# Kernel optimization log

Hardware: AMD Instinct MI355X
Metric: run time of the kernel (lower is better)

## Reference

```python
import jax, jax.numpy as jnp
import numpy as np

HID = 768
INTER = 3072
H = 12
DH = 64
N = 16384
W = 256   # attention_width
L = 512   # per-sequence length (power of 2, used via the uint32 bit-mask trick)


def rotate_every_two(x):
    x1 = x[..., ::2]
    x2 = x[..., 1::2]
    return jnp.stack((-x2, x1), axis=-1).reshape(x.shape)


def setup_inputs() -> dict:
    key = jax.random.key(0)
    ks = jax.random.split(key, 6)
    # GPT-J style interleaved rotary tables: sin/cos each value repeated twice
    inv_freq = 1.0 / (10000.0 ** (np.arange(0, DH, 2) / DH))  # [DH/2]
    ang = np.arange(N)[:, None] * inv_freq[None, :]           # [N, DH/2]
    pos_sin = jnp.asarray(np.repeat(np.sin(ang), 2, axis=-1), dtype=jnp.float32)
    pos_cos = jnp.asarray(np.repeat(np.cos(ang), 2, axis=-1), dtype=jnp.float32)
    return {
        "x": jax.random.normal(ks[0], (N, HID), dtype=jnp.float32),
        "normed_ages": jax.random.normal(ks[1], (N,), dtype=jnp.float32),
        "pos_sin": pos_sin,
        "pos_cos": pos_cos,
        "ln_scale": jnp.ones((HID,), dtype=jnp.float32),
        "ln_offset": jnp.zeros((HID,), dtype=jnp.float32),
        "w_in": jax.random.normal(ks[2], (HID, 3 * HID + INTER), dtype=jnp.float32) * 0.02,
        "b_in": jnp.zeros((3 * HID + INTER,), dtype=jnp.float32),
        "w_out": jax.random.normal(ks[3], (HID + INTER, HID), dtype=jnp.float32) * 0.02,
        "b_out": jnp.zeros((HID,), dtype=jnp.float32),
        "length": L,
    }


def reference(x, normed_ages, pos_sin, pos_cos, ln_scale, ln_offset,
              w_in, b_in, w_out, b_out, length):
    # LayerNorm (haiku: eps=1e-5, create_scale/offset)
    mu = jnp.mean(x, axis=-1, keepdims=True)
    var = jnp.var(x, axis=-1, keepdims=True)
    xn = (x - mu) * jax.lax.rsqrt(var + 1e-5) * ln_scale + ln_offset

    # fused QKV + FF projection (note: original computes x_with_ages but never uses it)
    mid = xn @ w_in + b_in
    q, k, v, ff = jnp.split(mid, [HID, 2 * HID, 3 * HID], axis=-1)

    def to_heads(t):  # [N, HID] -> [H, N, DH]
        return t.reshape(N, H, DH).transpose(1, 0, 2)

    q, k, v = to_heads(q), to_heads(k), to_heads(v)

    # rotary ('per_head'): sincos broadcast over heads
    sin, cos = pos_sin[None], pos_cos[None]
    q = q * cos + rotate_every_two(q) * sin
    k = k * cos + rotate_every_two(k) * sin

    # local (sliding-window, causal, within-sequence) attention, chunked by W
    C = W
    nc = N // C
    qc = q.reshape(H, nc, C, DH)
    kc = k.reshape(H, nc, C, DH)
    vc = v.reshape(H, nc, C, DH)
    kprev = jnp.concatenate([jnp.zeros_like(kc[:, :1]), kc[:, :-1]], axis=1)
    vprev = jnp.concatenate([jnp.zeros_like(vc[:, :1]), vc[:, :-1]], axis=1)
    kcat = jnp.concatenate([kprev, kc], axis=2)  # [H, nc, 2C, DH]
    vcat = jnp.concatenate([vprev, vc], axis=2)

    qi = (jnp.arange(nc) * C)[:, None] + jnp.arange(C)        # [nc, C]
    kj = (jnp.arange(nc) * C)[:, None] - C + jnp.arange(2 * C)  # [nc, 2C]
    lm = ~(jnp.uint32(length) - jnp.uint32(1))  # same bit-trick as the module
    same_seq = ((qi[:, :, None].astype(jnp.uint32) & lm) ==
                (jnp.maximum(kj, 0)[:, None, :].astype(jnp.uint32) & lm))
    d = qi[:, :, None] - kj[:, None, :]
    mask = (kj[:, None, :] >= 0) & (d >= 0) & (d < W) & same_seq  # [nc, C, 2C]

    scale = 1.0 / jnp.sqrt(jnp.float32(DH))
    scores = jnp.einsum('hncd,hnkd->hnck', qc, kcat) * scale
    scores = jnp.where(mask[None], scores, jnp.float32(-1e30))
    probs = jax.nn.softmax(scores, axis=-1)
    attn = jnp.einsum('hnck,hnkd->hncd', probs, vcat)

    attn = attn.reshape(H, N, DH).transpose(1, 0, 2).reshape(N, HID)
    combined = jnp.concatenate([attn, jax.nn.gelu(ff)], axis=-1)
    return xn + combined @ w_out + b_out
```

## Files before the change

kernel.cpp:

```cpp
#include <hip/hip_runtime.h>

#define N_TOK 16384
#define HIDN  768
#define MIDN  5376
#define COMBN 3840
#define NH    12
#define DHD   64
#define CHUNK 256
#define WIN   256

typedef short s16x8 __attribute__((ext_vector_type(8)));
typedef short s16x4 __attribute__((ext_vector_type(4)));
typedef float f32x4 __attribute__((ext_vector_type(4)));

__device__ __forceinline__ float bf2f(unsigned short u){
  union { unsigned u; float f; } x; x.u = ((unsigned)u) << 16; return x.f;
}
__device__ __forceinline__ unsigned short f2bf(float f){
  union { float f; unsigned u; } x; x.f = f;
  unsigned r = x.u + 0x7fffu + ((x.u >> 16) & 1u);
  return (unsigned short)(r >> 16);
}
__device__ __forceinline__ float gelu_fast(float x){
  float u = -1.5957691216057308f * (x + 0.044715f * x * x * x);
  return x / (1.f + __expf(u));
}
__device__ __forceinline__ void glds16(const void* g, void* l){
  __builtin_amdgcn_global_load_lds(
      (const __attribute__((address_space(1))) unsigned*)g,
      (__attribute__((address_space(3))) unsigned*)l, 16, 0, 0);
}

__global__ __launch_bounds__(256) void transpose_f2b(
    const float* __restrict__ in, unsigned short* __restrict__ out,
    int R, int Cc)
{
  __shared__ short t[64 * 72];
  const int tid = threadIdx.x;
  const int r0 = blockIdx.y * 64, c0 = blockIdx.x * 64;
  #pragma unroll
  for (int rep = 0; rep < 4; rep++){
    int v = tid + 256 * rep;
    int r = v >> 4, s = v & 15;
    float4 d = *(const float4*)(in + (size_t)(r0 + r) * Cc + c0 + s * 4);
    s16x4 o = { (short)f2bf(d.x), (short)f2bf(d.y), (short)f2bf(d.z), (short)f2bf(d.w) };
    *(s16x4*)(t + r * 72 + s * 4) = o;
  }
  __syncthreads();
  #pragma unroll
  for (int rep = 0; rep < 2; rep++){
    int v = tid + 256 * rep;
    int c = v & 63, s2 = v >> 6;
    s16x8 d;
    #pragma unroll
    for (int j = 0; j < 8; j++) d[j] = t[(s2 * 8 + j) * 72 + c];
    *(s16x8*)(out + (size_t)(c0 + c) * R + r0 + s2 * 8) = d;
  }
}

__global__ __launch_bounds__(256) void ln_kernel(
    const float* __restrict__ x, const float* __restrict__ sc,
    const float* __restrict__ ofs, unsigned short* __restrict__ xn)
{
  const int lane = threadIdx.x & 63, wv = threadIdx.x >> 6;
  const int row = blockIdx.x * 4 + wv;
  const float4* xr = (const float4*)(x + (size_t)row * HIDN);
  float4 vals[3];
  float sum = 0.f, sq = 0.f;
  #pragma unroll
  for (int j = 0; j < 3; j++){
    vals[j] = xr[lane + 64 * j];
    sum += vals[j].x + vals[j].y + vals[j].z + vals[j].w;
    sq  += vals[j].x * vals[j].x + vals[j].y * vals[j].y
         + vals[j].z * vals[j].z + vals[j].w * vals[j].w;
  }
  #pragma unroll
  for (int o = 1; o < 64; o <<= 1){ sum += __shfl_xor(sum, o); sq += __shfl_xor(sq, o); }
  const float mu = sum * (1.f / HIDN);
  const float rs = rsqrtf(fmaxf(sq * (1.f / HIDN) - mu * mu, 0.f) + 1e-5f);
  s16x4* xo = (s16x4*)(xn + (size_t)row * HIDN);
  const float4* scp = (const float4*)sc;
  const float4* ofp = (const float4*)ofs;
  #pragma unroll
  for (int j = 0; j < 3; j++){
    int p = lane + 64 * j;
    float4 s = scp[p], o = ofp[p];
    s16x4 w;
    w[0] = (short)f2bf((vals[j].x - mu) * rs * s.x + o.x);
    w[1] = (short)f2bf((vals[j].y - mu) * rs * s.y + o.y);
    w[2] = (short)f2bf((vals[j].z - mu) * rs * s.z + o.z);
    w[3] = (short)f2bf((vals[j].w - mu) * rs * s.w + o.w);
    xo[p] = w;
  }
}

template<int K>
__device__ __forceinline__ void gemm_pipe3(
    const unsigned short* __restrict__ A, const unsigned short* __restrict__ BT,
    short* SM,
    int tid, int quad, int l15, int wr, int wc, int m0, int n0,
    f32x4 acc[4][4])
{
  constexpr int T = K / 32;
  char* const SMc = (char*)SM;
  const int srow = tid >> 2;
  const int ksw  = ((tid & 3) ^ ((tid >> 3) & 3)) * 8;
  const unsigned short* Ap = A  + (size_t)(m0 + srow) * K + ksw;
  const unsigned short* Bp = BT + (size_t)(n0 + srow) * K + ksw;
  const size_t hstep = (size_t)64 * K;

  const int segx = ((quad ^ ((l15 >> 1) & 3)) << 4);
  int offA[4], offB[4];
  #pragma unroll
  for (int mf = 0; mf < 4; mf++) offA[mf] = (wr * 64 + mf * 16 + l15) * 64 + segx;
  #pragma unroll
  for (int nf = 0; nf < 4; nf++) offB[nf] = (wc * 64 + nf * 16 + l15) * 64 + segx;

  auto stage = [&](int tt){
    const int b = tt & 3;
    char* Ad = SMc + b * 16384 + tid * 16;
    char* Bd = SMc + b * 16384 + 8192 + tid * 16;
    glds16(Ap + tt * 32,         Ad);
    glds16(Ap + tt * 32 + hstep, Ad + 4096);
    glds16(Bp + tt * 32,         Bd);
    glds16(Bp + tt * 32 + hstep, Bd + 4096);
  };

  s16x8 af[4], bf[4];
  auto rdfrags = [&](int b){
    const char* Ab = SMc + b * 16384;
    const char* Bb = SMc + b * 16384 + 8192;
    #pragma unroll
    for (int i = 0; i < 4; i++) af[i] = *(const s16x8*)(Ab + offA[i]);
    #pragma unroll
    for (int j = 0; j < 4; j++) bf[j] = *(const s16x8*)(Bb + offB[j]);
  };

  stage(0); stage(1); stage(2); stage(3);
  asm volatile("s_waitcnt vmcnt(12)" ::: "memory");
  asm volatile("s_barrier" ::: "memory");
  rdfrags(0);

  #pragma unroll 4
  for (int t = 0; t < T; ++t){
    if (t + 4 < T) stage(t + 4);
    __builtin_amdgcn_s_setprio(1);
    #pragma unroll
    for (int i = 0; i < 4; i++)
      #pragma unroll
      for (int j = 0; j < 4; j++)
        acc[i][j] = __builtin_amdgcn_mfma_f32_16x16x32_bf16(af[i], bf[j], acc[i][j], 0, 0, 0);
    __builtin_amdgcn_s_setprio(0);
    if (t + 1 < T){
      if (t + 4 < T)      { asm volatile("s_waitcnt vmcnt(12)" ::: "memory"); }
      else if (t + 3 < T) { asm volatile("s_waitcnt vmcnt(8)"  ::: "memory"); }
      else if (t + 2 < T) { asm volatile("s_waitcnt vmcnt(4)"  ::: "memory"); }
      else                { asm volatile("s_waitcnt vmcnt(0)"  ::: "memory"); }
      asm volatile("s_barrier" ::: "memory");
      rdfrags((t + 1) & 3);
    }
  }
}

__global__ __launch_bounds__(256, 2) void gemm1_k(
    const unsigned short* __restrict__ A, const unsigned short* __restrict__ BT,
    const float* __restrict__ bias,
    const float* __restrict__ psin, const float* __restrict__ pcos,
    unsigned short* __restrict__ qb, unsigned short* __restrict__ kb,
    unsigned short* __restrict__ vb, unsigned short* __restrict__ comb)
{
  __shared__ short SM[32768];
  const int tid = threadIdx.x, lane = tid & 63, wv = tid >> 6;
  const int quad = lane >> 4, l15 = lane & 15;
  const int wr = wv >> 1, wc = wv & 1;

  const int nbx = gridDim.x;
  const int bid = blockIdx.x + blockIdx.y * nbx;
  const int GM = 16;
  const int group = bid / (GM * nbx);
  const int rem   = bid % (GM * nbx);
  const int m0 = (group * GM + (rem % GM)) * 128;
  const int n0 = (rem / GM) * 128;

  f32x4 acc[4][4];
  #pragma unroll
  for (int i = 0; i < 4; i++)
    #pragma unroll
    for (int j = 0; j < 4; j++) acc[i][j] = (f32x4){0.f,0.f,0.f,0.f};

  gemm_pipe3<HIDN>(A, BT, SM, tid, quad, l15, wr, wc, m0, n0, acc);

  unsigned short* dstb; int cb; int cls;
  if (n0 < 768)       { dstb = qb;   cb = n0;        cls = 0; }
  else if (n0 < 1536) { dstb = kb;   cb = n0 - 768;  cls = 1; }
  else if (n0 < 2304) { dstb = vb;   cb = n0 - 1536; cls = 2; }
  else                { dstb = comb; cb = n0 - 1536; cls = 3; }
  const int rowstride = (cls == 3) ? COMBN : HIDN;

  float bsv[4];
  #pragma unroll
  for (int nf = 0; nf < 4; nf++) bsv[nf] = bias[n0 + wc * 64 + nf * 16 + l15];

  if (cls <= 1){
    const float qscale = (cls == 0) ? 0.125f : 1.0f;
    #pragma unroll
    for (int mf = 0; mf < 4; mf++){
      #pragma unroll
      for (int r = 0; r < 4; r++){
        const int row = m0 + wr * 64 + mf * 16 + quad * 4 + r;
        unsigned short* rp = dstb + (size_t)row * rowstride + cb + wc * 64;
        const float* sp = psin + (size_t)row * DHD;
        const float* cp = pcos + (size_t)row * DHD;
        #pragma unroll
        for (int nf = 0; nf < 4; nf++){
          const int d = nf * 16 + l15;
          float v = acc[mf][nf][r] + bsv[nf];
          float vp = __shfl_xor(v, 1);
          const float s = sp[d], c = cp[d];
          float o = (l15 & 1) ? (v * c + vp * s) : (v * c - vp * s);
          rp[d] = f2bf(o * qscale);
        }
      }
    }
  } else {
    #pragma unroll
    for (int mf = 0; mf < 4; mf++){
      #pragma unroll
      for (int r = 0; r < 4; r++){
        const int row = m0 + wr * 64 + mf * 16 + quad * 4 + r;
        unsigned short* rp = dstb + (size_t)row * rowstride + cb + wc * 64;
        #pragma unroll
        for (int nf = 0; nf < 4; nf++){
          float val = acc[mf][nf][r] + bsv[nf];
          if (cls == 3) val = gelu_fast(val);
          rp[nf * 16 + l15] = f2bf(val);
        }
      }
    }
  }
}

__global__ __launch_bounds__(256, 2) void gemm2_k(
    const unsigned short* __restrict__ A, const unsigned short* __restrict__ BT,
    const float* __restrict__ bias, const unsigned short* __restrict__ xn,
    float* __restrict__ outp)
{
  __shared__ short SM[32768];
  const int tid = threadIdx.x, lane = tid & 63, wv = tid >> 6;
  const int quad = lane >> 4, l15 = lane & 15;
  const int wr = wv >> 1, wc = wv & 1;
  const int n0 = blockIdx.x * 128, m0 = blockIdx.y * 128;

  f32x4 acc[4][4];
  #pragma unroll
  for (int i = 0; i < 4; i++)
    #pragma unroll
    for (int j = 0; j < 4; j++) acc[i][j] = (f32x4){0.f,0.f,0.f,0.f};

  gemm_pipe3<COMBN>(A, BT, SM, tid, quad, l15, wr, wc, m0, n0, acc);

  float bsv[4];
  #pragma unroll
  for (int nf = 0; nf < 4; nf++) bsv[nf] = bias[n0 + wc * 64 + nf * 16 + l15];

  #pragma unroll
  for (int mf = 0; mf < 4; mf++){
    #pragma unroll
    for (int r = 0; r < 4; r++){
      const int row = m0 + wr * 64 + mf * 16 + quad * 4 + r;
      const size_t rb = (size_t)row * HIDN + n0 + wc * 64;
      #pragma unroll
      for (int nf = 0; nf < 4; nf++){
        const size_t o = rb + nf * 16 + l15;
        outp[o] = bf2f(xn[o]) + acc[mf][nf][r] + bsv[nf];
      }
    }
  }
}

__global__ __launch_bounds__(256) void attn_kernel(
    const unsigned short* __restrict__ qb, const unsigned short* __restrict__ kb,
    const unsigned short* __restrict__ vb, unsigned short* __restrict__ comb,
    const int* __restrict__ lenp)
{
  __shared__ short Ks[2][64 * 72];
  __shared__ short Vt[2][64 * 64];
  __shared__ short Ps[4][16 * 72];
  const int tid = threadIdx.x, lane = tid & 63, wv = tid >> 6;
  const int quad = lane >> 4, l15 = lane & 15;
  const int h = blockIdx.y, c = blockIdx.x;
  const unsigned lm = ~((unsigned)lenp[0] - 1u);
  const int i0 = c * CHUNK + wv * 64;
  const unsigned short* qh = qb + h * DHD;
  const unsigned short* kh = kb + h * DHD;
  const unsigned short* vh = vb + h * DHD;

  s16x8 qf[4][2];
  #pragma unroll
  for (int rt = 0; rt < 4; rt++){
    const unsigned short* qr = qh + (size_t)(i0 + rt * 16 + l15) * HIDN;
    qf[rt][0] = *(const s16x8*)(qr + quad * 8);
    qf[rt][1] = *(const s16x8*)(qr + 32 + quad * 8);
  }

  f32x4 O[4][4];
  float mm[4][4], ll[4][4];
  #pragma unroll
  for (int rt = 0; rt < 4; rt++)
    #pragma unroll
    for (int j = 0; j < 4; j++){ O[rt][j] = (f32x4){0,0,0,0}; mm[rt][j] = -1e30f; ll[rt][j] = 0.f; }
  short* myP = &Ps[wv][0];

  const int skey = tid & 63, sseg = tid >> 6;
  const int jb0 = c * CHUNK - 256;
  s16x8 kr[2], vr[2];

  auto issue = [&](int jb){
    if (jb >= 0){
      const unsigned short* kp = kh + (size_t)(jb + skey) * HIDN + sseg * 16;
      const unsigned short* vp = vh + (size_t)(jb + skey) * HIDN + sseg * 16;
      kr[0] = *(const s16x8*)(kp);     kr[1] = *(const s16x8*)(kp + 8);
      vr[0] = *(const s16x8*)(vp);     vr[1] = *(const s16x8*)(vp + 8);
    } else {
      kr[0] = kr[1] = vr[0] = vr[1] = (s16x8){0,0,0,0,0,0,0,0};
    }
  };

  issue(jb0);
  for (int tb = 0; tb < 8; tb++){
    const int jb = jb0 + tb * 64;
    const int buf = tb & 1;
    short* Kb = &Ks[buf][0];
    short* Vb = &Vt[buf][0];
    *(s16x8*)(Kb + skey * 72 + sseg * 16)     = kr[0];
    *(s16x8*)(Kb + skey * 72 + sseg * 16 + 8) = kr[1];
    #pragma unroll
    for (int half = 0; half < 2; half++)
      #pragma unroll
      for (int j = 0; j < 8; j++){
        const int d = sseg * 16 + half * 8 + j;
        Vb[d * 64 + (((skey & 56) ^ ((d & 7) << 3)) | (skey & 7))] = vr[half][j];
      }
    if (tb < 7) issue(jb + 64);
    __syncthreads();

    const bool act = (jb >= 0) && (jb <= i0 + 63) && (jb + 63 >= i0 - 255) &&
                     (((unsigned)i0 & lm) == ((unsigned)jb & lm));
    if (!act) continue;

    #pragma unroll
    for (int rt = 0; rt < 4; rt++){
      const int ilo = i0 + rt * 16;
      if (ilo + 15 < jb || ilo - (jb + 63) >= WIN) continue;
      f32x4 sc[4];
      #pragma unroll
      for (int ct = 0; ct < 4; ct++){
        const short* kbase = Kb + (ct * 16 + l15) * 72 + quad * 8;
        const s16x8 b0 = *(const s16x8*)(kbase);
        const s16x8 b1 = *(const s16x8*)(kbase + 32);
        f32x4 aa = (f32x4){0,0,0,0};
        aa = __builtin_amdgcn_mfma_f32_16x16x32_bf16(qf[rt][0], b0, aa, 0, 0, 0);
        aa = __builtin_amdgcn_mfma_f32_16x16x32_bf16(qf[rt][1], b1, aa, 0, 0, 0);
        sc[ct] = aa;
      }
      float alph[4];
      #pragma unroll
      for (int r = 0; r < 4; r++){
        const int i = ilo + quad * 4 + r;
        #pragma unroll
        for (int ct = 0; ct < 4; ct++){
          const unsigned dd = (unsigned)(i - (jb + ct * 16 + l15));
          if (dd >= 256u) sc[ct][r] = -1e30f;
        }
        float mx = fmaxf(fmaxf(sc[0][r], sc[1][r]), fmaxf(sc[2][r], sc[3][r]));
        mx = fmaxf(mx, __shfl_xor(mx, 1));
        mx = fmaxf(mx, __shfl_xor(mx, 2));
        mx = fmaxf(mx, __shfl_xor(mx, 4));
        mx = fmaxf(mx, __shfl_xor(mx, 8));
        const float mnew = fmaxf(mm[rt][r], mx);
        alph[r] = __expf(mm[rt][r] - mnew);
        mm[rt][r] = mnew;
        float p0 = __expf(sc[0][r] - mnew);
        float p1 = __expf(sc[1][r] - mnew);
        float p2 = __expf(sc[2][r] - mnew);
        float p3 = __expf(sc[3][r] - mnew);
        sc[0][r] = p0; sc[1][r] = p1; sc[2][r] = p2; sc[3][r] = p3;
        float rsum = (p0 + p1) + (p2 + p3);
        rsum += __shfl_xor(rsum, 1);
        rsum += __shfl_xor(rsum, 2);
        rsum += __shfl_xor(rsum, 4);
        rsum += __shfl_xor(rsum, 8);
        ll[rt][r] = ll[rt][r] * alph[r] + rsum;
      }
      #pragma unroll
      for (int co = 0; co < 4; co++)
        #pragma unroll
        for (int r = 0; r < 4; r++) O[rt][co][r] *= alph[r];
      #pragma unroll
      for (int r = 0; r < 4; r++){
        const int prow = quad * 4 + r;
        #pragma unroll
        for (int ct = 0; ct < 4; ct++)
          myP[prow * 72 + ct * 16 + l15] = (short)f2bf(sc[ct][r]);
      }
      #pragma unroll
      for (int ks2 = 0; ks2 < 2; ks2++){
        const s16x8 pf = *(const s16x8*)(myP + l15 * 72 + ks2 * 32 + quad * 8);
        #pragma unroll
        for (int co = 0; co < 4; co++){
          const int d = co * 16 + l15;
          const s16x8 vf = *(const s16x8*)(Vb + d * 64 +
                              ((ks2 * 32 + quad * 8) ^ ((d & 7) << 3)));
          O[rt][co] = __builtin_amdgcn_mfma_f32_16x16x32_bf16(pf, vf, O[rt][co], 0, 0, 0);
        }
      }
    }
  }

  #pragma unroll
  for (int rt = 0; rt < 4; rt++)
    #pragma unroll
    for (int co = 0; co < 4; co++)
      #pragma unroll
      for (int r = 0; r < 4; r++){
        const int tok = i0 + rt * 16 + quad * 4 + r;
        comb[(size_t)tok * COMBN + h * DHD + co * 16 + l15] = f2bf(O[rt][co][r] / ll[rt][r]);
      }
}

extern "C" void kernel_launch(void* const* d_in, const int* in_sizes, int n_in,
                              void* d_out, int out_size, void* d_ws, size_t ws_size,
                              hipStream_t stream)
{
  const float* x     = (const float*)d_in[0];
  const float* psin  = (const float*)d_in[2];
  const float* pcos  = (const float*)d_in[3];
  const float* lns   = (const float*)d_in[4];
  const float* lno   = (const float*)d_in[5];
  const float* w_in  = (const float*)d_in[6];
  const float* b_in  = (const float*)d_in[7];
  const float* w_out = (const float*)d_in[8];
  const float* b_out = (const float*)d_in[9];
  const int*   lenp  = (const int*)d_in[10];
  float* out = (float*)d_out;

  char* ws = (char*)d_ws;
  size_t off = 0;
  unsigned short* xn    = (unsigned short*)(ws + off); off += (size_t)N_TOK * HIDN * 2;
  unsigned short* wInT  = (unsigned short*)(ws + off); off += (size_t)MIDN * HIDN * 2;
  unsigned short* wOutT = (unsigned short*)(ws + off); off += (size_t)HIDN * COMBN * 2;
  unsigned short* qbuf  = (unsigned short*)(ws + off); off += (size_t)N_TOK * HIDN * 2;
  unsigned short* kbuf  = (unsigned short*)(ws + off); off += (size_t)N_TOK * HIDN * 2;
  unsigned short* vbuf  = (unsigned short*)(ws + off); off += (size_t)N_TOK * HIDN * 2;
  unsigned short* comb  = (unsigned short*)(ws + off); off += (size_t)N_TOK * COMBN * 2;

  transpose_f2b<<<dim3(MIDN/64, HIDN/64), 256, 0, stream>>>(w_in, wInT, HIDN, MIDN);
  transpose_f2b<<<dim3(HIDN/64, COMBN/64), 256, 0, stream>>>(w_out, wOutT, COMBN, HIDN);
  ln_kernel<<<dim3(N_TOK/4), 256, 0, stream>>>(x, lns, lno, xn);
  gemm1_k<<<dim3(MIDN/128, N_TOK/128), 256, 0, stream>>>(
      xn, wInT, b_in, psin, pcos, qbuf, kbuf, vbuf, comb);
  attn_kernel<<<dim3(N_TOK/CHUNK, NH), 256, 0, stream>>>(
      qbuf, kbuf, vbuf, comb, lenp);
  gemm2_k<<<dim3(HIDN/128, N_TOK/128), 256, 0, stream>>>(
      comb, wOutT, b_out, xn, out);
}
```

Baseline: 608.4 us.

## Widen GEMM tiles to 128x256 with a three-buffer LDS pipeline

Both GEMM kernels now compute a 128x256 output tile per block instead of 128x128, so each wave holds a 4x8 MFMA accumulator grid. The aim is more reuse of each loaded A fragment and fewer redundant global and LDS loads of A. The LDS pipeline drops from four 16KB stages to three 24KB stages, and the prefetch of the next stage now issues after the barrier so the buffer being overwritten is known to be free. The epilogues (rotary, GELU, residual) are remapped to the wider tile. In exchange, accumulator register pressure doubles, prefetch depth is shorter, and the output-projection GEMM launches only half as many blocks, which may underfill the GPU.

```diff
diff --git a/kernel.cpp b/kernel.cpp
--- a/kernel.cpp
+++ b/kernel.cpp
@@ -95,11 +95,11 @@
 }
 
 template<int K>
-__device__ __forceinline__ void gemm_pipe3(
+__device__ __forceinline__ void gemm_pipe4(
     const unsigned short* __restrict__ A, const unsigned short* __restrict__ BT,
     short* SM,
     int tid, int quad, int l15, int wr, int wc, int m0, int n0,
-    f32x4 acc[4][4])
+    f32x4 acc[4][8])
 {
   constexpr int T = K / 32;
   char* const SMc = (char*)SM;
@@ -107,57 +107,57 @@
   const int ksw  = ((tid & 3) ^ ((tid >> 3) & 3)) * 8;
   const unsigned short* Ap = A  + (size_t)(m0 + srow) * K + ksw;
   const unsigned short* Bp = BT + (size_t)(n0 + srow) * K + ksw;
-  const size_t hstep = (size_t)64 * K;
+  const size_t rstep = (size_t)64 * K;
 
   const int segx = ((quad ^ ((l15 >> 1) & 3)) << 4);
-  int offA[4], offB[4];
+  int offA[4], offB[8];
   #pragma unroll
   for (int mf = 0; mf < 4; mf++) offA[mf] = (wr * 64 + mf * 16 + l15) * 64 + segx;
   #pragma unroll
-  for (int nf = 0; nf < 4; nf++) offB[nf] = (wc * 64 + nf * 16 + l15) * 64 + segx;
+  for (int nf = 0; nf < 8; nf++) offB[nf] = 8192 + (wc * 128 + nf * 16 + l15) * 64 + segx;
 
   auto stage = [&](int tt){
-    const int b = tt & 3;
-    char* Ad = SMc + b * 16384 + tid * 16;
-    char* Bd = SMc + b * 16384 + 8192 + tid * 16;
-    glds16(Ap + tt * 32,         Ad);
-    glds16(Ap + tt * 32 + hstep, Ad + 4096);
-    glds16(Bp + tt * 32,         Bd);
-    glds16(Bp + tt * 32 + hstep, Bd + 4096);
+    const int b = tt % 3;
+    char* Ad = SMc + b * 24576 + tid * 16;
+    char* Bd = SMc + b * 24576 + 8192 + tid * 16;
+    const unsigned short* As = Ap + tt * 32;
+    const unsigned short* Bs = Bp + tt * 32;
+    glds16(As,         Ad);
+    glds16(As + rstep, Ad + 4096);
+    #pragma unroll
+    for (int r = 0; r < 4; r++)
+      glds16(Bs + r * rstep, Bd + r * 4096);
   };
 
-  s16x8 af[4], bf[4];
+  s16x8 af[4], bf[8];
   auto rdfrags = [&](int b){
-    const char* Ab = SMc + b * 16384;
-    const char* Bb = SMc + b * 16384 + 8192;
-    #pragma unroll
-    for (int i = 0; i < 4; i++) af[i] = *(const s16x8*)(Ab + offA[i]);
-    #pragma unroll
-    for (int j = 0; j < 4; j++) bf[j] = *(const s16x8*)(Bb + offB[j]);
+    const char* Bb = SMc + b * 24576;
+    #pragma unroll
+    for (int i = 0; i < 4; i++) af[i] = *(const s16x8*)(Bb + offA[i]);
+    #pragma unroll
+    for (int j = 0; j < 8; j++) bf[j] = *(const s16x8*)(Bb + offB[j]);
   };
 
-  stage(0); stage(1); stage(2); stage(3);
+  stage(0); stage(1); stage(2);
   asm volatile("s_waitcnt vmcnt(12)" ::: "memory");
   asm volatile("s_barrier" ::: "memory");
   rdfrags(0);
 
-  #pragma unroll 4
+  #pragma unroll 3
   for (int t = 0; t < T; ++t){
-    if (t + 4 < T) stage(t + 4);
     __builtin_amdgcn_s_setprio(1);
     #pragma unroll
     for (int i = 0; i < 4; i++)
       #pragma unroll
-      for (int j = 0; j < 4; j++)
+      for (int j = 0; j < 8; j++)
         acc[i][j] = __builtin_amdgcn_mfma_f32_16x16x32_bf16(af[i], bf[j], acc[i][j], 0, 0, 0);
     __builtin_amdgcn_s_setprio(0);
     if (t + 1 < T){
-      if (t + 4 < T)      { asm volatile("s_waitcnt vmcnt(12)" ::: "memory"); }
-      else if (t + 3 < T) { asm volatile("s_waitcnt vmcnt(8)"  ::: "memory"); }
-      else if (t + 2 < T) { asm volatile("s_waitcnt vmcnt(4)"  ::: "memory"); }
-      else                { asm volatile("s_waitcnt vmcnt(0)"  ::: "memory"); }
+      if (t + 2 < T){ asm volatile("s_waitcnt vmcnt(6)" ::: "memory"); }
+      else          { asm volatile("s_waitcnt vmcnt(0)" ::: "memory"); }
       asm volatile("s_barrier" ::: "memory");
-      rdfrags((t + 1) & 3);
+      rdfrags((t + 1) % 3);
+      if (t + 3 < T) stage(t + 3);
     }
   }
 }
@@ -169,7 +169,7 @@
     unsigned short* __restrict__ qb, unsigned short* __restrict__ kb,
     unsigned short* __restrict__ vb, unsigned short* __restrict__ comb)
 {
-  __shared__ short SM[32768];
+  __shared__ short SM[36864];
   const int tid = threadIdx.x, lane = tid & 63, wv = tid >> 6;
   const int quad = lane >> 4, l15 = lane & 15;
   const int wr = wv >> 1, wc = wv & 1;
@@ -180,15 +180,15 @@
   const int group = bid / (GM * nbx);
   const int rem   = bid % (GM * nbx);
   const int m0 = (group * GM + (rem % GM)) * 128;
-  const int n0 = (rem / GM) * 128;
-
-  f32x4 acc[4][4];
+  const int n0 = (rem / GM) * 256;
+
+  f32x4 acc[4][8];
   #pragma unroll
   for (int i = 0; i < 4; i++)
     #pragma unroll
-    for (int j = 0; j < 4; j++) acc[i][j] = (f32x4){0.f,0.f,0.f,0.f};
-
-  gemm_pipe3<HIDN>(A, BT, SM, tid, quad, l15, wr, wc, m0, n0, acc);
+    for (int j = 0; j < 8; j++) acc[i][j] = (f32x4){0.f,0.f,0.f,0.f};
+
+  gemm_pipe4<HIDN>(A, BT, SM, tid, quad, l15, wr, wc, m0, n0, acc);
 
   unsigned short* dstb; int cb; int cls;
   if (n0 < 768)       { dstb = qb;   cb = n0;        cls = 0; }
@@ -197,9 +197,9 @@
   else                { dstb = comb; cb = n0 - 1536; cls = 3; }
   const int rowstride = (cls == 3) ? COMBN : HIDN;
 
-  float bsv[4];
-  #pragma unroll
-  for (int nf = 0; nf < 4; nf++) bsv[nf] = bias[n0 + wc * 64 + nf * 16 + l15];
+  float bsv[8];
+  #pragma unroll
+  for (int nf = 0; nf < 8; nf++) bsv[nf] = bias[n0 + wc * 128 + nf * 16 + l15];
 
   if (cls <= 1){
     const float qscale = (cls == 0) ? 0.125f : 1.0f;
@@ -208,17 +208,17 @@
       #pragma unroll
       for (int r = 0; r < 4; r++){
         const int row = m0 + wr * 64 + mf * 16 + quad * 4 + r;
-        unsigned short* rp = dstb + (size_t)row * rowstride + cb + wc * 64;
+        unsigned short* rp = dstb + (size_t)row * rowstride + cb + wc * 128;
         const float* sp = psin + (size_t)row * DHD;
         const float* cp = pcos + (size_t)row * DHD;
         #pragma unroll
-        for (int nf = 0; nf < 4; nf++){
-          const int d = nf * 16 + l15;
+        for (int nf = 0; nf < 8; nf++){
+          const int d = (nf & 3) * 16 + l15;
           float v = acc[mf][nf][r] + bsv[nf];
           float vp = __shfl_xor(v, 1);
           const float s = sp[d], c = cp[d];
           float o = (l15 & 1) ? (v * c + vp * s) : (v * c - vp * s);
-          rp[d] = f2bf(o * qscale);
+          rp[nf * 16 + l15] = f2bf(o * qscale);
         }
       }
     }
@@ -228,9 +228,9 @@
       #pragma unroll
       for (int r = 0; r < 4; r++){
         const int row = m0 + wr * 64 + mf * 16 + quad * 4 + r;
-        unsigned short* rp = dstb + (size_t)row * rowstride + cb + wc * 64;
-        #pragma unroll
-        for (int nf = 0; nf < 4; nf++){
+        unsigned short* rp = dstb + (size_t)row * rowstride + cb + wc * 128;
+        #pragma unroll
+        for (int nf = 0; nf < 8; nf++){
           float val = acc[mf][nf][r] + bsv[nf];
           if (cls == 3) val = gelu_fast(val);
           rp[nf * 16 + l15] = f2bf(val);
@@ -245,32 +245,32 @@
     const float* __restrict__ bias, const unsigned short* __restrict__ xn,
     float* __restrict__ outp)
 {
-  __shared__ short SM[32768];
+  __shared__ short SM[36864];
   const int tid = threadIdx.x, lane = tid & 63, wv = tid >> 6;
   const int quad = lane >> 4, l15 = lane & 15;
   const int wr = wv >> 1, wc = wv & 1;
-  const int n0 = blockIdx.x * 128, m0 = blockIdx.y * 128;
-
-  f32x4 acc[4][4];
+  const int n0 = blockIdx.x * 256, m0 = blockIdx.y * 128;
+
+  f32x4 acc[4][8];
   #pragma unroll
   for (int i = 0; i < 4; i++)
     #pragma unroll
-    for (int j = 0; j < 4; j++) acc[i][j] = (f32x4){0.f,0.f,0.f,0.f};
-
-  gemm_pipe3<COMBN>(A, BT, SM, tid, quad, l15, wr, wc, m0, n0, acc);
-
-  float bsv[4];
-  #pragma unroll
-  for (int nf = 0; nf < 4; nf++) bsv[nf] = bias[n0 + wc * 64 + nf * 16 + l15];
+    for (int j = 0; j < 8; j++) acc[i][j] = (f32x4){0.f,0.f,0.f,0.f};
+
+  gemm_pipe4<COMBN>(A, BT, SM, tid, quad, l15, wr, wc, m0, n0, acc);
+
+  float bsv[8];
+  #pragma unroll
+  for (int nf = 0; nf < 8; nf++) bsv[nf] = bias[n0 + wc * 128 + nf * 16 + l15];
 
   #pragma unroll
   for (int mf = 0; mf < 4; mf++){
     #pragma unroll
     for (int r = 0; r < 4; r++){
       const int row = m0 + wr * 64 + mf * 16 + quad * 4 + r;
-      const size_t rb = (size_t)row * HIDN + n0 + wc * 64;
-      #pragma unroll
-      for (int nf = 0; nf < 4; nf++){
+      const size_t rb = (size_t)row * HIDN + n0 + wc * 128;
+      #pragma unroll
+      for (int nf = 0; nf < 8; nf++){
         const size_t o = rb + nf * 16 + l15;
         outp[o] = bf2f(xn[o]) + acc[mf][nf][r] + bsv[nf];
       }
@@ -457,10 +457,10 @@
   transpose_f2b<<<dim3(MIDN/64, HIDN/64), 256, 0, stream>>>(w_in, wInT, HIDN, MIDN);
   transpose_f2b<<<dim3(HIDN/64, COMBN/64), 256, 0, stream>>>(w_out, wOutT, COMBN, HIDN);
   ln_kernel<<<dim3(N_TOK/4), 256, 0, stream>>>(x, lns, lno, xn);
-  gemm1_k<<<dim3(MIDN/128, N_TOK/128), 256, 0, stream>>>(
+  gemm1_k<<<dim3(MIDN/256, N_TOK/128), 256, 0, stream>>>(
       xn, wInT, b_in, psin, pcos, qbuf, kbuf, vbuf, comb);
   attn_kernel<<<dim3(N_TOK/CHUNK, NH), 256, 0, stream>>>(
       qbuf, kbuf, vbuf, comb, lenp);
-  gemm2_k<<<dim3(HIDN/128, N_TOK/128), 256, 0, stream>>>(
+  gemm2_k<<<dim3(HIDN/256, N_TOK/128), 256, 0, stream>>>(
       comb, wOutT, b_out, xn, out);
 }
```

Measured after the change: 581.1 us. 1.05x faster.
